# Performance work log

Hardware: AMD Instinct MI355X
Metric: run time of the kernel (lower is better)

The kernel has to match this reference:

```python
import jax, jax.numpy as jnp
import numpy as np

K = 8          # num groups / object slots
FC = 256       # fc_size
LAST = 128     # last_fc_size
B = 2048       # batch
M = 1024       # input size
H = 512        # state (hidden) size


def _ln(x, g, b):
    # LayerNorm over last dim, eps matches torch default 1e-5
    mu = jnp.mean(x, axis=-1, keepdims=True)
    var = jnp.mean((x - mu) ** 2, axis=-1, keepdims=True)
    return (x - mu) * jax.lax.rsqrt(var + 1e-5) * g + b


def setup_inputs() -> dict:
    key = jax.random.key(0)
    ks = jax.random.split(key, 10)
    s = 0.05
    d = {
        "x": jax.random.normal(ks[0], (B * K, M), jnp.float32),
        "state": jax.random.normal(ks[1], (B * K, H), jnp.float32),
        # encoder: Linear(H->FC) + LN(FC)
        "enc_w": jax.random.normal(ks[2], (H, FC), jnp.float32) * s,
        "enc_b": jnp.zeros((FC,), jnp.float32),
        "enc_g": jnp.ones((FC,), jnp.float32),
        "enc_bb": jnp.zeros((FC,), jnp.float32),
        # core: Linear(2*FC->FC) + LN(FC)
        "core_w": jax.random.normal(ks[3], (2 * FC, FC), jnp.float32) * s,
        "core_b": jnp.zeros((FC,), jnp.float32),
        "core_g": jnp.ones((FC,), jnp.float32),
        "core_bb": jnp.zeros((FC,), jnp.float32),
        # context: Linear(FC->FC) + LN(FC)
        "ctx_w": jax.random.normal(ks[4], (FC, FC), jnp.float32) * s,
        "ctx_b": jnp.zeros((FC,), jnp.float32),
        "ctx_g": jnp.ones((FC,), jnp.float32),
        "ctx_bb": jnp.zeros((FC,), jnp.float32),
        # attention: Linear(FC->LAST) + LN(LAST) + Tanh + Linear(LAST->1) + Sigmoid
        "att1_w": jax.random.normal(ks[5], (FC, LAST), jnp.float32) * s,
        "att1_b": jnp.zeros((LAST,), jnp.float32),
        "att_g": jnp.ones((LAST,), jnp.float32),
        "att_bb": jnp.zeros((LAST,), jnp.float32),
        "att2_w": jax.random.normal(ks[6], (LAST, 1), jnp.float32) * s,
        "att2_b": jnp.zeros((1,), jnp.float32),
        # out_fc: Linear(FC + FC + M -> FC)
        "out_w": jax.random.normal(ks[7], (FC + FC + M, FC), jnp.float32) * s,
        "out_b": jnp.zeros((FC,), jnp.float32),
    }
    return d


def reference(x, state, enc_w, enc_b, enc_g, enc_bb,
              core_w, core_b, core_g, core_bb,
              ctx_w, ctx_b, ctx_g, ctx_bb,
              att1_w, att1_b, att_g, att_bb, att2_w, att2_b,
              out_w, out_b):
    bk, m = x.shape
    k = K
    b = bk // k
    # 0. encode state: [B*K, H] -> [B*K, FC]
    s1 = jax.nn.relu(_ln(state @ enc_w + enc_b, enc_g, enc_bb))
    h1 = s1.shape[-1]
    s1r = s1.reshape(b, k, h1)
    # focus: K-1 copies of each slot's state  [b, k, k-1, h1]
    fs = jnp.broadcast_to(s1r[:, :, None, :], (b, k, k - 1, h1))
    # context: gather the K-1 other slots' states (replaces torch python loop)
    idx = np.array([[j for j in range(k) if j != i] for i in range(k)])  # [k, k-1]
    cs = s1r[:, idx, :]  # [b, k, k-1, h1]
    concat = jnp.concatenate([fs, cs], axis=-1).reshape(b * k * (k - 1), 2 * h1)
    # core / context MLPs over pairs
    core = jax.nn.relu(_ln(concat @ core_w + core_b, core_g, core_bb))   # [b*k*(k-1), FC]
    ctx = jax.nn.relu(_ln(core @ ctx_w + ctx_b, ctx_g, ctx_bb))          # [b*k*(k-1), FC]
    # attention scalar per pair
    att_h = jnp.tanh(_ln(core @ att1_w + att1_b, att_g, att_bb))
    att = jax.nn.sigmoid(att_h @ att2_w + att2_b)                        # [b*k*(k-1), 1]
    # attention-weighted sum over the K-1 context dim
    h2 = ctx.shape[-1]
    effect = jnp.sum(ctx.reshape(b * k, k - 1, h2) * att.reshape(b * k, k - 1, 1), axis=1)
    # decode: concat encoded state, effect, input -> new state
    total = jnp.concatenate([s1, effect, x], axis=-1)
    new_state = total @ out_w + out_b
    return (new_state, new_state)
```

## Files before the change

kernel.cpp:

```cpp
#include <hip/hip_runtime.h>
#include <stdint.h>

#define FC    256
#define HH    512
#define MX    1024
#define LASTN 128
#define NROW  16384
#define NGRP  2048

typedef unsigned short u16;
typedef __bf16 bf16x8 __attribute__((ext_vector_type(8)));
typedef float  f32x4  __attribute__((ext_vector_type(4)));

__device__ __forceinline__ float red16(float v) {
#pragma unroll
  for (int m = 1; m < 16; m <<= 1) v += __shfl_xor(v, m);
  return v;
}
__device__ __forceinline__ u16 to_bf16(float f) {
  unsigned u = __float_as_uint(f);
  return (u16)((u + 0x8000u) >> 16);
}
__device__ __forceinline__ float from_bf16(u16 s) {
  return __uint_as_float(((unsigned)s) << 16);
}
__device__ __forceinline__ uint32_t pk2(float a, float b) {
  return (uint32_t)to_bf16(a) | ((uint32_t)to_bf16(b) << 16);
}
__device__ __forceinline__ float tanh_fast(float x) {
  float e = __expf(2.f * x);
  return __fdividef(e - 1.f, e + 1.f);
}
__device__ __forceinline__ float sigmoid_fast(float x) {
  return __fdividef(1.f, 1.f + __expf(-x));
}
__device__ __forceinline__ void glds16(const void* g, void* l) {
  __builtin_amdgcn_global_load_lds(
      (__attribute__((address_space(1))) uint32_t*)g,
      (__attribute__((address_space(3))) uint32_t*)l, 16, 0, 0);
}
__device__ __forceinline__ bf16x8 frag_ld(const u16* p) {
  return __builtin_bit_cast(bf16x8, *(const uint4*)p);
}

__global__ __launch_bounds__(256) void k_prep(
    const float* __restrict__ enc_w, const float* __restrict__ core_w,
    const float* __restrict__ ctx_w, const float* __restrict__ att1_w,
    const float* __restrict__ out_w,
    u16* __restrict__ encT, u16* __restrict__ uvT, u16* __restrict__ ctxT,
    u16* __restrict__ attT, u16* __restrict__ outT)
{
  const int bx = blockIdx.x, tid = threadIdx.x;
  const float* W; u16* D; int NKC, N, local; int uv = 0;
  if (bx < 64)       { W = enc_w;  D = encT; NKC = 16; N = 256; local = bx * 256 + tid; }
  else if (bx < 128) { W = core_w; D = uvT;  NKC = 8;  N = 256; local = (bx-64)*256 + tid; uv = 1; }
  else if (bx < 160) { W = ctx_w;  D = ctxT; NKC = 8;  N = 256; local = (bx-128)*256 + tid; }
  else if (bx < 176) { W = att1_w; D = attT; NKC = 8;  N = 128; local = (bx-160)*256 + tid; }
  else               { W = out_w;  D = outT; NKC = 48; N = 256; local = (bx-176)*256 + tid; }
  const int l  = local & 63;
  const int kc = (local >> 6) % NKC;
  const int u  = (local >> 6) / NKC;
  const int n  = u * 16 + (l & 15);
  const int k0 = kc * 32 + (l >> 4) * 8;
  float f[8];
#pragma unroll
  for (int j = 0; j < 8; ++j) {
    const int k = k0 + j;
    if (uv) f[j] = (n < 256) ? W[(size_t)k * 256 + n] : W[(size_t)(256 + k) * 256 + (n - 256)];
    else    f[j] = W[(size_t)k * N + n];
  }
  uint4 w;
  w.x = pk2(f[0], f[1]); w.y = pk2(f[2], f[3]);
  w.z = pk2(f[4], f[5]); w.w = pk2(f[6], f[7]);
  *(uint4*)&D[(size_t)local * 8] = w;
}

__global__ __launch_bounds__(256) void k_enc(
    const float* __restrict__ state, const u16* __restrict__ encT,
    const float* __restrict__ enc_b, const float* __restrict__ enc_g,
    const float* __restrict__ enc_bb, u16* __restrict__ s1b)
{
  __shared__ __align__(16) u16 smA[128 * 8];
  __shared__ __align__(16) u16 smB[16 * 64 * 8];
  __shared__ float smP[2][2][16][2];
  const int tid = threadIdx.x, wv = tid >> 6, lane = tid & 63;
  const int cl = lane & 15, quad = lane >> 4;
  const int rb = wv >> 1, cb = wv & 1;
  const int row0 = blockIdx.x * 32;
  f32x4 acc[8];
#pragma unroll
  for (int u = 0; u < 8; ++u) acc[u] = (f32x4){0.f, 0.f, 0.f, 0.f};

  for (int kc = 0; kc < 16; ++kc) {
    __syncthreads();
    if (tid < 128) {
      const int rblk = tid >> 6, ll = tid & 63;
      const float* src = state + (size_t)(row0 + rblk * 16 + (ll & 15)) * HH + kc * 32 + (ll >> 4) * 8;
      float4 a = *(const float4*)src, b = *(const float4*)(src + 4);
      uint4 w; w.x = pk2(a.x, a.y); w.y = pk2(a.z, a.w); w.z = pk2(b.x, b.y); w.w = pk2(b.z, b.w);
      *(uint4*)&smA[(size_t)tid * 8] = w;
    }
#pragma unroll
    for (int i = 0; i < 4; ++i) {
      const int u = wv * 4 + i;
      glds16(encT + ((size_t)(u * 16 + kc) * 64 + lane) * 8, &smB[u * 512]);
    }
    __syncthreads();
    bf16x8 af = frag_ld(&smA[(rb * 64 + lane) * 8]);
#pragma unroll
    for (int u = 0; u < 8; ++u) {
      bf16x8 bf = frag_ld(&smB[((cb * 8 + u) * 64 + lane) * 8]);
      acc[u] = __builtin_amdgcn_mfma_f32_16x16x32_bf16(af, bf, acc[u], 0, 0, 0);
    }
  }
  float bias[8], gg[8], bb[8];
#pragma unroll
  for (int u = 0; u < 8; ++u) {
    const int col = cb * 128 + u * 16 + cl;
    bias[u] = enc_b[col]; gg[u] = enc_g[col]; bb[u] = enc_bb[col];
  }
  float vv[4][8];
#pragma unroll
  for (int r4 = 0; r4 < 4; ++r4) {
    float s = 0.f, sq = 0.f;
#pragma unroll
    for (int u = 0; u < 8; ++u) {
      float v = acc[u][r4] + bias[u];
      vv[r4][u] = v; s += v; sq += v * v;
    }
    s = red16(s); sq = red16(sq);
    if (cl == 0) { smP[cb][rb][quad * 4 + r4][0] = s; smP[cb][rb][quad * 4 + r4][1] = sq; }
  }
  __syncthreads();
#pragma unroll
  for (int r4 = 0; r4 < 4; ++r4) {
    const int rr = quad * 4 + r4;
    const float S  = smP[0][rb][rr][0] + smP[1][rb][rr][0];
    const float SQ = smP[0][rb][rr][1] + smP[1][rb][rr][1];
    const float mu = S * (1.f / 256.f);
    const float rs = rsqrtf(SQ * (1.f / 256.f) - mu * mu + 1e-5f);
    const int row = row0 + rb * 16 + rr;
#pragma unroll
    for (int u = 0; u < 8; ++u) {
      float o = fmaxf((vv[r4][u] - mu) * rs * gg[u] + bb[u], 0.f);
      s1b[(size_t)row * FC + cb * 128 + u * 16 + cl] = to_bf16(o);
    }
  }
}

__global__ __launch_bounds__(256) void k_uv(
    const u16* __restrict__ s1b, const u16* __restrict__ uvT,
    float* __restrict__ UV)
{
  __shared__ __align__(16) u16 smA[4 * 64 * 8];
  __shared__ __align__(16) u16 smB[8 * 64 * 8];
  const int tid = threadIdx.x, wv = tid >> 6, lane = tid & 63;
  const int cl = lane & 15, quad = lane >> 4;
  const int row0 = blockIdx.x * 64;
  const int nb = blockIdx.y;
  f32x4 acc[8];
#pragma unroll
  for (int u = 0; u < 8; ++u) acc[u] = (f32x4){0.f, 0.f, 0.f, 0.f};

  for (int kc = 0; kc < 8; ++kc) {
    __syncthreads();
    glds16(s1b + (size_t)(row0 + wv * 16 + (lane & 15)) * FC + kc * 32 + (lane >> 4) * 8,
           &smA[wv * 512]);
#pragma unroll
    for (int i = 0; i < 2; ++i) {
      const int u = wv * 2 + i;
      glds16(uvT + ((size_t)((nb * 8 + u) * 8 + kc) * 64 + lane) * 8, &smB[u * 512]);
    }
    __syncthreads();
    bf16x8 af = frag_ld(&smA[(wv * 64 + lane) * 8]);
#pragma unroll
    for (int u = 0; u < 8; ++u) {
      bf16x8 bf = frag_ld(&smB[(u * 64 + lane) * 8]);
      acc[u] = __builtin_amdgcn_mfma_f32_16x16x32_bf16(af, bf, acc[u], 0, 0, 0);
    }
  }
#pragma unroll
  for (int r4 = 0; r4 < 4; ++r4) {
    const int row = row0 + wv * 16 + quad * 4 + r4;
#pragma unroll
    for (int u = 0; u < 8; ++u)
      UV[(size_t)row * 512 + nb * 128 + u * 16 + cl] = acc[u][r4];
  }
}

__global__ __launch_bounds__(256, 3) void k_pair(
    const float* __restrict__ UV, const float* __restrict__ core_b,
    const float* __restrict__ core_g, const float* __restrict__ core_bb,
    const u16* __restrict__ ctxT, const float* __restrict__ ctx_b,
    const float* __restrict__ ctx_g, const float* __restrict__ ctx_bb,
    const u16* __restrict__ attT, const float* __restrict__ att1_b,
    const float* __restrict__ att_g, const float* __restrict__ att_bb,
    const float* __restrict__ att2_w, const float* __restrict__ att2_b,
    u16* __restrict__ effb)
{
  __shared__ __align__(16) u16 smA[2048 * 8];
  __shared__ __align__(16) u16 smB[16 * 64 * 8];
  __shared__ float att_s[64];
  const int g = blockIdx.x;
  const int tid = threadIdx.x, wv = tid >> 6, lane = tid & 63;
  const int cl = lane & 15, quad = lane >> 4;

#pragma unroll
  for (int i = 0; i < 8; ++i)
    *(uint4*)&smA[(size_t)(tid + i * 256) * 8] = (uint4){0u, 0u, 0u, 0u};
  __syncthreads();

  {
    const int sub = lane >> 4, cl16 = lane & 15;
    const int c0 = cl16 * 16;
    float4 CB[4], CG[4], CBB[4];
#pragma unroll
    for (int q = 0; q < 4; ++q) {
      CB[q]  = *(const float4*)&core_b[c0 + q * 4];
      CG[q]  = *(const float4*)&core_g[c0 + q * 4];
      CBB[q] = *(const float4*)&core_bb[c0 + q * 4];
    }
#pragma unroll
    for (int it = 0; it < 4; ++it) {
      const int p = it * 16 + wv * 4 + sub;
      if (p < 56) {
        const int i = p / 7, t = p - i * 7;
        const int j = t + (t >= i ? 1 : 0);
        const float* uA = UV + (size_t)(g * 8 + i) * 512 + c0;
        const float* vB = UV + (size_t)(g * 8 + j) * 512 + 256 + c0;
        float v[16];
        float s = 0.f, sq = 0.f;
#pragma unroll
        for (int q = 0; q < 4; ++q) {
          float4 ua = *(const float4*)(uA + q * 4);
          float4 vb = *(const float4*)(vB + q * 4);
          float x0 = ua.x + vb.x + CB[q].x, x1 = ua.y + vb.y + CB[q].y;
          float x2 = ua.z + vb.z + CB[q].z, x3 = ua.w + vb.w + CB[q].w;
          v[q*4+0] = x0; v[q*4+1] = x1; v[q*4+2] = x2; v[q*4+3] = x3;
          s += x0 + x1 + x2 + x3;
          sq += x0*x0 + x1*x1 + x2*x2 + x3*x3;
        }
        s = red16(s); sq = red16(sq);
        const float mu = s * (1.f / 256.f);
        const float rs = rsqrtf(sq * (1.f / 256.f) - mu * mu + 1e-5f);
        float o[16];
#pragma unroll
        for (int q = 0; q < 4; ++q) {
          o[q*4+0] = fmaxf((v[q*4+0] - mu) * rs * CG[q].x + CBB[q].x, 0.f);
          o[q*4+1] = fmaxf((v[q*4+1] - mu) * rs * CG[q].y + CBB[q].y, 0.f);
          o[q*4+2] = fmaxf((v[q*4+2] - mu) * rs * CG[q].z + CBB[q].z, 0.f);
          o[q*4+3] = fmaxf((v[q*4+3] - mu) * rs * CG[q].w + CBB[q].w, 0.f);
        }
        const int base = ((p >> 4) * 8 + (cl16 >> 1)) * 64;
        const int lane1 = (p & 15) + 16 * ((cl16 & 1) * 2);
        uint4 w1, w2;
        w1.x = pk2(o[0], o[1]);  w1.y = pk2(o[2], o[3]);
        w1.z = pk2(o[4], o[5]);  w1.w = pk2(o[6], o[7]);
        w2.x = pk2(o[8], o[9]);  w2.y = pk2(o[10], o[11]);
        w2.z = pk2(o[12], o[13]); w2.w = pk2(o[14], o[15]);
        *(uint4*)&smA[(size_t)(base + lane1) * 8] = w1;
        *(uint4*)&smA[(size_t)(base + lane1 + 16) * 8] = w2;
      }
    }
  }
  __syncthreads();

  f32x4 accC[16], accT[8];
#pragma unroll
  for (int t = 0; t < 16; ++t) accC[t] = (f32x4){0.f, 0.f, 0.f, 0.f};
#pragma unroll
  for (int t = 0; t < 8; ++t)  accT[t] = (f32x4){0.f, 0.f, 0.f, 0.f};

  for (int kc = 0; kc < 8; ++kc) {
    if (kc) __syncthreads();
#pragma unroll
    for (int i = 0; i < 4; ++i) {
      const int q = wv * 4 + i;
      glds16(ctxT + ((size_t)(q * 8 + kc) * 64 + lane) * 8, &smB[q * 512]);
    }
    uint4 attf[8];
#pragma unroll
    for (int q = 0; q < 8; ++q)
      attf[q] = *(const uint4*)(attT + ((size_t)(q * 8 + kc) * 64 + lane) * 8);
    __syncthreads();
    bf16x8 af = frag_ld(&smA[((wv * 8 + kc) * 64 + lane) * 8]);
#pragma unroll
    for (int q = 0; q < 16; ++q) {
      bf16x8 bf = frag_ld(&smB[(q * 64 + lane) * 8]);
      accC[q] = __builtin_amdgcn_mfma_f32_16x16x32_bf16(af, bf, accC[q], 0, 0, 0);
    }
#pragma unroll
    for (int q = 0; q < 8; ++q) {
      bf16x8 bf = __builtin_bit_cast(bf16x8, attf[q]);
      accT[q] = __builtin_amdgcn_mfma_f32_16x16x32_bf16(af, bf, accT[q], 0, 0, 0);
    }
  }

  {
    float ab[8], ag[8], abb[8], aw[8];
#pragma unroll
    for (int t = 0; t < 8; ++t) {
      const int col = t * 16 + cl;
      ab[t] = att1_b[col]; ag[t] = att_g[col]; abb[t] = att_bb[col]; aw[t] = att2_w[col];
    }
    const float b2 = att2_b[0];
#pragma unroll
    for (int r4 = 0; r4 < 4; ++r4) {
      float v[8], s = 0.f, sq = 0.f;
#pragma unroll
      for (int t = 0; t < 8; ++t) {
        v[t] = accT[t][r4] + ab[t];
        s += v[t]; sq += v[t] * v[t];
      }
      s = red16(s); sq = red16(sq);
      const float mu = s * (1.f / 128.f);
      const float rs = rsqrtf(sq * (1.f / 128.f) - mu * mu + 1e-5f);
      float d = 0.f;
#pragma unroll
      for (int t = 0; t < 8; ++t) {
        float h = tanh_fast((v[t] - mu) * rs * ag[t] + abb[t]);
        d = fmaf(h, aw[t], d);
      }
      d = red16(d);
      if (cl == 0) {
        const int r = wv * 16 + quad * 4 + r4;
        if (r < 56) att_s[r] = sigmoid_fast(d + b2);
      }
    }
  }
  __syncthreads();

  u16* smS = smA;
  {
    float cb[16], cg[16], cbb[16];
#pragma unroll
    for (int t = 0; t < 16; ++t) {
      const int col = t * 16 + cl;
      cb[t] = ctx_b[col]; cg[t] = ctx_g[col]; cbb[t] = ctx_bb[col];
    }
#pragma unroll
    for (int r4 = 0; r4 < 4; ++r4) {
      float v[16], s = 0.f, sq = 0.f;
#pragma unroll
      for (int t = 0; t < 16; ++t) {
        v[t] = accC[t][r4] + cb[t];
        s += v[t]; sq += v[t] * v[t];
      }
      s = red16(s); sq = red16(sq);
      const float mu = s * (1.f / 256.f);
      const float rs = rsqrtf(sq * (1.f / 256.f) - mu * mu + 1e-5f);
      const int r = wv * 16 + quad * 4 + r4;
      if (r < 56) {
        const float ap = att_s[r];
#pragma unroll
        for (int t = 0; t < 16; ++t) {
          const int col = t * 16 + cl;
          float o = fmaxf((v[t] - mu) * rs * cg[t] + cbb[t], 0.f) * ap;
          smS[r * 264 + col] = to_bf16(o);
        }
      }
    }
  }
  __syncthreads();

  const int c = tid;
#pragma unroll
  for (int i = 0; i < 8; ++i) {
    float s = 0.f;
#pragma unroll
    for (int t2 = 0; t2 < 7; ++t2) s += from_bf16(smS[(i * 7 + t2) * 264 + c]);
    effb[(size_t)(g * 8 + i) * FC + c] = to_bf16(s);
  }
}

__global__ __launch_bounds__(256) void k_out(
    const u16* __restrict__ s1b, const u16* __restrict__ effb,
    const float* __restrict__ x, const u16* __restrict__ outT,
    const float* __restrict__ out_b, float* __restrict__ out, int dup)
{
  __shared__ __align__(16) u16 smA[4 * 64 * 8];
  __shared__ __align__(16) u16 smB[8 * 64 * 8];
  const int tid = threadIdx.x, wv = tid >> 6, lane = tid & 63;
  const int cl = lane & 15, quad = lane >> 4;
  const int row0 = blockIdx.x * 64;
  const int nb = blockIdx.y;
  f32x4 acc[8];
#pragma unroll
  for (int u = 0; u < 8; ++u) acc[u] = (f32x4){0.f, 0.f, 0.f, 0.f};

  for (int kc = 0; kc < 48; ++kc) {
    __syncthreads();
    if (kc < 16) {
      const u16* base = (kc < 8) ? s1b : effb;
      const int kof = (kc & 7) * 32;
      glds16(base + (size_t)(row0 + wv * 16 + (lane & 15)) * FC + kof + (lane >> 4) * 8,
             &smA[wv * 512]);
    } else {
      const int t = tid >> 6, ll = tid & 63;
      const float* src = x + (size_t)(row0 + t * 16 + (ll & 15)) * MX + (kc - 16) * 32 + (ll >> 4) * 8;
      float4 a = *(const float4*)src, b = *(const float4*)(src + 4);
      uint4 w; w.x = pk2(a.x, a.y); w.y = pk2(a.z, a.w); w.z = pk2(b.x, b.y); w.w = pk2(b.z, b.w);
      *(uint4*)&smA[(size_t)tid * 8] = w;
    }
#pragma unroll
    for (int i = 0; i < 2; ++i) {
      const int u = wv * 2 + i;
      glds16(outT + ((size_t)((nb * 8 + u) * 48 + kc) * 64 + lane) * 8, &smB[u * 512]);
    }
    __syncthreads();
    bf16x8 af = frag_ld(&smA[(wv * 64 + lane) * 8]);
#pragma unroll
    for (int u = 0; u < 8; ++u) {
      bf16x8 bf = frag_ld(&smB[(u * 64 + lane) * 8]);
      acc[u] = __builtin_amdgcn_mfma_f32_16x16x32_bf16(af, bf, acc[u], 0, 0, 0);
    }
  }
  float bias[8];
#pragma unroll
  for (int u = 0; u < 8; ++u) bias[u] = out_b[nb * 128 + u * 16 + cl];
#pragma unroll
  for (int r4 = 0; r4 < 4; ++r4) {
    const int row = row0 + wv * 16 + quad * 4 + r4;
#pragma unroll
    for (int u = 0; u < 8; ++u) {
      const float o = acc[u][r4] + bias[u];
      const size_t off = (size_t)row * FC + nb * 128 + u * 16 + cl;
      out[off] = o;
      if (dup) out[(size_t)NROW * FC + off] = o;
    }
  }
}

extern "C" void kernel_launch(void* const* d_in, const int* in_sizes, int n_in,
                              void* d_out, int out_size, void* d_ws, size_t ws_size,
                              hipStream_t stream) {
  const float* x      = (const float*)d_in[0];
  const float* state  = (const float*)d_in[1];
  const float* enc_w  = (const float*)d_in[2];
  const float* enc_b  = (const float*)d_in[3];
  const float* enc_g  = (const float*)d_in[4];
  const float* enc_bb = (const float*)d_in[5];
  const float* core_w = (const float*)d_in[6];
  const float* core_b = (const float*)d_in[7];
  const float* core_g = (const float*)d_in[8];
  const float* core_bb= (const float*)d_in[9];
  const float* ctx_w  = (const float*)d_in[10];
  const float* ctx_b  = (const float*)d_in[11];
  const float* ctx_g  = (const float*)d_in[12];
  const float* ctx_bb = (const float*)d_in[13];
  const float* att1_w = (const float*)d_in[14];
  const float* att1_b = (const float*)d_in[15];
  const float* att_g  = (const float*)d_in[16];
  const float* att_bb = (const float*)d_in[17];
  const float* att2_w = (const float*)d_in[18];
  const float* att2_b = (const float*)d_in[19];
  const float* out_w  = (const float*)d_in[20];
  const float* out_b  = (const float*)d_in[21];

  char* ws = (char*)d_ws;
  float* UV  = (float*)ws;
  u16* s1b   = (u16*)(ws + 33554432);
  u16* effb  = (u16*)(ws + 41943040);
  u16* encT  = (u16*)(ws + 50331648);
  u16* uvT   = (u16*)(ws + 50593792);
  u16* ctxT  = (u16*)(ws + 50855936);
  u16* attT  = (u16*)(ws + 50987008);
  u16* outT  = (u16*)(ws + 51052544);
  float* out = (float*)d_out;
  const int dup = (out_size >= 2 * NROW * FC) ? 1 : 0;

  k_prep<<<dim3(368), 256, 0, stream>>>(enc_w, core_w, ctx_w, att1_w, out_w,
                                        encT, uvT, ctxT, attT, outT);
  k_enc<<<dim3(NROW / 32), 256, 0, stream>>>(state, encT, enc_b, enc_g, enc_bb, s1b);
  k_uv <<<dim3(NROW / 64, 4), 256, 0, stream>>>(s1b, uvT, UV);
  k_pair<<<dim3(NGRP), 256, 0, stream>>>(UV, core_b, core_g, core_bb,
                                         ctxT, ctx_b, ctx_g, ctx_bb,
                                         attT, att1_b, att_g, att_bb,
                                         att2_w, att2_b, effb);
  k_out<<<dim3(NROW / 64, 2), 256, 0, stream>>>(s1b, effb, x, outT, out_b, out, dup);
}
```

Before: 345.1 us.

## Double K-step per barrier in GEMM kernels and stage UV rows in LDS

```diff
diff --git a/kernel.cpp b/kernel.cpp
--- a/kernel.cpp
+++ b/kernel.cpp
@@ -80,8 +80,8 @@
     const float* __restrict__ enc_b, const float* __restrict__ enc_g,
     const float* __restrict__ enc_bb, u16* __restrict__ s1b)
 {
-  __shared__ __align__(16) u16 smA[128 * 8];
-  __shared__ __align__(16) u16 smB[16 * 64 * 8];
+  __shared__ __align__(16) u16 smA[2][128 * 8];
+  __shared__ __align__(16) u16 smB[2][16 * 64 * 8];
   __shared__ float smP[2][2][16][2];
   const int tid = threadIdx.x, wv = tid >> 6, lane = tid & 63;
   const int cl = lane & 15, quad = lane >> 4;
@@ -91,26 +91,33 @@
 #pragma unroll
   for (int u = 0; u < 8; ++u) acc[u] = (f32x4){0.f, 0.f, 0.f, 0.f};
 
-  for (int kc = 0; kc < 16; ++kc) {
-    __syncthreads();
-    if (tid < 128) {
-      const int rblk = tid >> 6, ll = tid & 63;
+  for (int kk = 0; kk < 8; ++kk) {
+    __syncthreads();
+    {
+      const int p = tid >> 7, lu = tid & 127;
+      const int kc = kk * 2 + p;
+      const int rblk = lu >> 6, ll = lu & 63;
       const float* src = state + (size_t)(row0 + rblk * 16 + (ll & 15)) * HH + kc * 32 + (ll >> 4) * 8;
       float4 a = *(const float4*)src, b = *(const float4*)(src + 4);
       uint4 w; w.x = pk2(a.x, a.y); w.y = pk2(a.z, a.w); w.z = pk2(b.x, b.y); w.w = pk2(b.z, b.w);
-      *(uint4*)&smA[(size_t)tid * 8] = w;
-    }
-#pragma unroll
-    for (int i = 0; i < 4; ++i) {
-      const int u = wv * 4 + i;
-      glds16(encT + ((size_t)(u * 16 + kc) * 64 + lane) * 8, &smB[u * 512]);
-    }
-    __syncthreads();
-    bf16x8 af = frag_ld(&smA[(rb * 64 + lane) * 8]);
-#pragma unroll
-    for (int u = 0; u < 8; ++u) {
-      bf16x8 bf = frag_ld(&smB[((cb * 8 + u) * 64 + lane) * 8]);
-      acc[u] = __builtin_amdgcn_mfma_f32_16x16x32_bf16(af, bf, acc[u], 0, 0, 0);
+      *(uint4*)&smA[p][(size_t)lu * 8] = w;
+    }
+#pragma unroll
+    for (int p = 0; p < 2; ++p)
+#pragma unroll
+      for (int i = 0; i < 4; ++i) {
+        const int u = wv * 4 + i;
+        glds16(encT + ((size_t)(u * 16 + kk * 2 + p) * 64 + lane) * 8, &smB[p][u * 512]);
+      }
+    __syncthreads();
+#pragma unroll
+    for (int p = 0; p < 2; ++p) {
+      bf16x8 af = frag_ld(&smA[p][(rb * 64 + lane) * 8]);
+#pragma unroll
+      for (int u = 0; u < 8; ++u) {
+        bf16x8 bf = frag_ld(&smB[p][((cb * 8 + u) * 64 + lane) * 8]);
+        acc[u] = __builtin_amdgcn_mfma_f32_16x16x32_bf16(af, bf, acc[u], 0, 0, 0);
+      }
     }
   }
   float bias[8], gg[8], bb[8];
@@ -152,8 +159,8 @@
     const u16* __restrict__ s1b, const u16* __restrict__ uvT,
     float* __restrict__ UV)
 {
-  __shared__ __align__(16) u16 smA[4 * 64 * 8];
-  __shared__ __align__(16) u16 smB[8 * 64 * 8];
+  __shared__ __align__(16) u16 smA[2][4 * 64 * 8];
+  __shared__ __align__(16) u16 smB[2][8 * 64 * 8];
   const int tid = threadIdx.x, wv = tid >> 6, lane = tid & 63;
   const int cl = lane & 15, quad = lane >> 4;
   const int row0 = blockIdx.x * 64;
@@ -162,21 +169,28 @@
 #pragma unroll
   for (int u = 0; u < 8; ++u) acc[u] = (f32x4){0.f, 0.f, 0.f, 0.f};
 
-  for (int kc = 0; kc < 8; ++kc) {
-    __syncthreads();
-    glds16(s1b + (size_t)(row0 + wv * 16 + (lane & 15)) * FC + kc * 32 + (lane >> 4) * 8,
-           &smA[wv * 512]);
-#pragma unroll
-    for (int i = 0; i < 2; ++i) {
-      const int u = wv * 2 + i;
-      glds16(uvT + ((size_t)((nb * 8 + u) * 8 + kc) * 64 + lane) * 8, &smB[u * 512]);
-    }
-    __syncthreads();
-    bf16x8 af = frag_ld(&smA[(wv * 64 + lane) * 8]);
-#pragma unroll
-    for (int u = 0; u < 8; ++u) {
-      bf16x8 bf = frag_ld(&smB[(u * 64 + lane) * 8]);
-      acc[u] = __builtin_amdgcn_mfma_f32_16x16x32_bf16(af, bf, acc[u], 0, 0, 0);
+  for (int kk = 0; kk < 4; ++kk) {
+    __syncthreads();
+#pragma unroll
+    for (int p = 0; p < 2; ++p) {
+      const int kc = kk * 2 + p;
+      glds16(s1b + (size_t)(row0 + wv * 16 + (lane & 15)) * FC + kc * 32 + (lane >> 4) * 8,
+             &smA[p][wv * 512]);
+#pragma unroll
+      for (int i = 0; i < 2; ++i) {
+        const int u = wv * 2 + i;
+        glds16(uvT + ((size_t)((nb * 8 + u) * 8 + kc) * 64 + lane) * 8, &smB[p][u * 512]);
+      }
+    }
+    __syncthreads();
+#pragma unroll
+    for (int p = 0; p < 2; ++p) {
+      bf16x8 af = frag_ld(&smA[p][(wv * 64 + lane) * 8]);
+#pragma unroll
+      for (int u = 0; u < 8; ++u) {
+        bf16x8 bf = frag_ld(&smB[p][(u * 64 + lane) * 8]);
+        acc[u] = __builtin_amdgcn_mfma_f32_16x16x32_bf16(af, bf, acc[u], 0, 0, 0);
+      }
     }
   }
 #pragma unroll
@@ -188,7 +202,7 @@
   }
 }
 
-__global__ __launch_bounds__(256, 3) void k_pair(
+__global__ __launch_bounds__(256, 2) void k_pair(
     const float* __restrict__ UV, const float* __restrict__ core_b,
     const float* __restrict__ core_g, const float* __restrict__ core_bb,
     const u16* __restrict__ ctxT, const float* __restrict__ ctx_b,
@@ -200,11 +214,19 @@
 {
   __shared__ __align__(16) u16 smA[2048 * 8];
   __shared__ __align__(16) u16 smB[16 * 64 * 8];
+  __shared__ __align__(16) float smUV[16 * 256];
   __shared__ float att_s[64];
   const int g = blockIdx.x;
   const int tid = threadIdx.x, wv = tid >> 6, lane = tid & 63;
   const int cl = lane & 15, quad = lane >> 4;
 
+#pragma unroll
+  for (int i = 0; i < 4; ++i) {
+    const int r = wv * 4 + i;
+    const int row = g * 8 + (r & 7);
+    const int half = r >> 3;
+    glds16(UV + (size_t)row * 512 + half * 256 + lane * 4, &smUV[r * 256]);
+  }
 #pragma unroll
   for (int i = 0; i < 8; ++i)
     *(uint4*)&smA[(size_t)(tid + i * 256) * 8] = (uint4){0u, 0u, 0u, 0u};
@@ -226,8 +248,8 @@
       if (p < 56) {
         const int i = p / 7, t = p - i * 7;
         const int j = t + (t >= i ? 1 : 0);
-        const float* uA = UV + (size_t)(g * 8 + i) * 512 + c0;
-        const float* vB = UV + (size_t)(g * 8 + j) * 512 + 256 + c0;
+        const float* uA = &smUV[i * 256 + c0];
+        const float* vB = &smUV[(8 + j) * 256 + c0];
         float v[16];
         float s = 0.f, sq = 0.f;
 #pragma unroll
@@ -378,8 +400,8 @@
     const float* __restrict__ x, const u16* __restrict__ outT,
     const float* __restrict__ out_b, float* __restrict__ out, int dup)
 {
-  __shared__ __align__(16) u16 smA[4 * 64 * 8];
-  __shared__ __align__(16) u16 smB[8 * 64 * 8];
+  __shared__ __align__(16) u16 smA[2][4 * 64 * 8];
+  __shared__ __align__(16) u16 smB[2][8 * 64 * 8];
   const int tid = threadIdx.x, wv = tid >> 6, lane = tid & 63;
   const int cl = lane & 15, quad = lane >> 4;
   const int row0 = blockIdx.x * 64;
@@ -388,31 +410,45 @@
 #pragma unroll
   for (int u = 0; u < 8; ++u) acc[u] = (f32x4){0.f, 0.f, 0.f, 0.f};
 
-  for (int kc = 0; kc < 48; ++kc) {
-    __syncthreads();
-    if (kc < 16) {
-      const u16* base = (kc < 8) ? s1b : effb;
-      const int kof = (kc & 7) * 32;
-      glds16(base + (size_t)(row0 + wv * 16 + (lane & 15)) * FC + kof + (lane >> 4) * 8,
-             &smA[wv * 512]);
+  for (int kk = 0; kk < 24; ++kk) {
+    const int kc0 = kk * 2;
+    __syncthreads();
+    if (kc0 < 16) {
+#pragma unroll
+      for (int p = 0; p < 2; ++p) {
+        const int kc = kc0 + p;
+        const u16* base = (kc < 8) ? s1b : effb;
+        const int kof = (kc & 7) * 32;
+        glds16(base + (size_t)(row0 + wv * 16 + (lane & 15)) * FC + kof + (lane >> 4) * 8,
+               &smA[p][wv * 512]);
+      }
     } else {
       const int t = tid >> 6, ll = tid & 63;
-      const float* src = x + (size_t)(row0 + t * 16 + (ll & 15)) * MX + (kc - 16) * 32 + (ll >> 4) * 8;
-      float4 a = *(const float4*)src, b = *(const float4*)(src + 4);
-      uint4 w; w.x = pk2(a.x, a.y); w.y = pk2(a.z, a.w); w.z = pk2(b.x, b.y); w.w = pk2(b.z, b.w);
-      *(uint4*)&smA[(size_t)tid * 8] = w;
-    }
-#pragma unroll
-    for (int i = 0; i < 2; ++i) {
-      const int u = wv * 2 + i;
-      glds16(outT + ((size_t)((nb * 8 + u) * 48 + kc) * 64 + lane) * 8, &smB[u * 512]);
-    }
-    __syncthreads();
-    bf16x8 af = frag_ld(&smA[(wv * 64 + lane) * 8]);
-#pragma unroll
-    for (int u = 0; u < 8; ++u) {
-      bf16x8 bf = frag_ld(&smB[(u * 64 + lane) * 8]);
-      acc[u] = __builtin_amdgcn_mfma_f32_16x16x32_bf16(af, bf, acc[u], 0, 0, 0);
+      const float* src0 = x + (size_t)(row0 + t * 16 + (ll & 15)) * MX + (ll >> 4) * 8;
+#pragma unroll
+      for (int p = 0; p < 2; ++p) {
+        const float* src = src0 + (kc0 + p - 16) * 32;
+        float4 a = *(const float4*)src, b = *(const float4*)(src + 4);
+        uint4 w; w.x = pk2(a.x, a.y); w.y = pk2(a.z, a.w); w.z = pk2(b.x, b.y); w.w = pk2(b.z, b.w);
+        *(uint4*)&smA[p][(size_t)tid * 8] = w;
+      }
+    }
+#pragma unroll
+    for (int p = 0; p < 2; ++p)
+#pragma unroll
+      for (int i = 0; i < 2; ++i) {
+        const int u = wv * 2 + i;
+        glds16(outT + ((size_t)((nb * 8 + u) * 48 + kc0 + p) * 64 + lane) * 8, &smB[p][u * 512]);
+      }
+    __syncthreads();
+#pragma unroll
+    for (int p = 0; p < 2; ++p) {
+      bf16x8 af = frag_ld(&smA[p][(wv * 64 + lane) * 8]);
+#pragma unroll
+      for (int u = 0; u < 8; ++u) {
+        bf16x8 bf = frag_ld(&smB[p][(u * 64 + lane) * 8]);
+        acc[u] = __builtin_amdgcn_mfma_f32_16x16x32_bf16(af, bf, acc[u], 0, 0, 0);
+      }
     }
   }
   float bias[8];
```

Result: faster. 303.6 us (-12.0%).
